# Kernel optimization log

Hardware: AMD Instinct MI355X
Metric: run time of the kernel (lower is better)

## Reference

```python
import jax, jax.numpy as jnp
import numpy as np

B, L_MAX, D, RL, RD, DOUT = 64, 4096, 128, 64, 16, 512
LN_EPS = 1e-5

def _xavier(key, shape):
    fan_in, fan_out = shape[0], shape[1]
    limit = np.sqrt(6.0 / (fan_in + fan_out)).astype(np.float32)
    return jax.random.uniform(key, shape, jnp.float32, -limit, limit)

def setup_inputs() -> dict:
    key = jax.random.key(0)
    ks = jax.random.split(key, 10)
    emb = jax.random.normal(ks[0], (B, L_MAX, D), jnp.float32)
    # contiguous padding mask from random true lengths (standard ESM padding)
    lengths = jax.random.randint(ks[1], (B,), 1, L_MAX + 1)
    mask = (jnp.arange(L_MAX)[None, :] < lengths[:, None])  # bool [B, L_max]
    B_c = _xavier(ks[2], (D, RD))
    A_c = _xavier(ks[3], (L_MAX, RL))
    H_c = _xavier(ks[4], (RL * RD, DOUT))
    W1 = _xavier(ks[5], (DOUT, DOUT))
    b1 = jnp.zeros((DOUT,), jnp.float32)
    ln_w = jnp.ones((DOUT,), jnp.float32)
    ln_b = jnp.zeros((DOUT,), jnp.float32)
    W2 = _xavier(ks[6], (DOUT, DOUT))
    b2 = jnp.zeros((DOUT,), jnp.float32)
    return {"emb": emb, "mask": mask, "B_c": B_c, "A_c": A_c, "H_c": H_c,
            "W1": W1, "b1": b1, "ln_w": ln_w, "ln_b": ln_b, "W2": W2, "b2": b2}

def reference(emb, mask, B_c, A_c, H_c, W1, b1, ln_w, ln_b, W2, b2):
    m = mask.astype(emb.dtype)                      # [B, L]
    X = emb * m[:, :, None]                         # masked embeddings [B, L, D]
    Y = jnp.einsum('bld,dr->blr', X, B_c)           # low-rank proj over D -> [B, L, rD]
    U = jnp.einsum('blr,lk->bkr', Y, A_c)           # low-rank proj over L -> [B, rL, rD]
    z = U.reshape(U.shape[0], -1) @ H_c             # [B, d]
    # expander: Linear -> LayerNorm -> ReLU -> Linear
    h = z @ W1 + b1
    mu = jnp.mean(h, axis=-1, keepdims=True)
    var = jnp.mean(jnp.square(h - mu), axis=-1, keepdims=True)
    h = (h - mu) / jnp.sqrt(var + LN_EPS) * ln_w + ln_b
    h = jax.nn.relu(h)
    return h @ W2 + b2
```

## Files before the change

kernel.cpp:

```cpp
#include <hip/hip_runtime.h>


__global__ __launch_bounds__(256) void detect_mask(
    const unsigned int* __restrict__ m, int* __restrict__ flag)
{
    unsigned int v = 0;
    int base = (blockIdx.x * 256 + threadIdx.x) * 4;
#pragma unroll
    for (int i = 0; i < 4; ++i) v |= m[base + i];
    unsigned long long any = __ballot(v > 1u);
    if ((threadIdx.x & 63) == 0 && any) atomicOr(flag, 1);
}

#define YS_STRIDE 20
#define BCS_CHUNK 516
__global__ __launch_bounds__(256, 4) void k1_proj(
    const float* __restrict__ emb,
    const void* __restrict__ maskp,
    const float* __restrict__ Bc,
    const float* __restrict__ Ac,
    float* __restrict__ Part,
    const int* __restrict__ flag)
{
    __shared__ __align__(16) float BcS[4 * BCS_CHUNK];
    __shared__ __align__(16) float As[64 * 64];
    __shared__ __align__(16) float Ys[64 * YS_STRIDE];

    const int tid  = threadIdx.x;
    const int lane = tid & 63;
    const int wave = tid >> 6;
    const int q    = tid & 3;
    const int r    = tid >> 2;
    const int b    = blockIdx.x >> 4;
    const int c    = blockIdx.x & 15;
    const int byte_mode = *flag;

#pragma unroll
    for (int i = 0; i < 8; ++i) {
        int e = i * 256 + tid;
        int k = e >> 4, col = e & 15;
        BcS[(k >> 5) * BCS_CHUNK + (k & 31) * 16 + col] = Bc[e];
    }
    __syncthreads();

    float accU[4] = {0.f, 0.f, 0.f, 0.f};

    for (int t = 0; t < 4; ++t) {
        const long l0 = (long)c * 256 + t * 64;
        const float* asrc = Ac + l0 * 64;

#pragma unroll
        for (int i = 0; i < 4; ++i) {
            int e = (i * 256 + tid) * 4;
            *(float4*)(As + e) = *(const float4*)(asrc + e);
        }

        const float* xrow = emb + ((long)b * 4096 + l0 + r) * 128 + q * 32;
        float4 xv[8];
#pragma unroll
        for (int j = 0; j < 8; ++j) xv[j] = *(const float4*)(xrow + j * 4);

        const float* bq = BcS + q * BCS_CHUNK;
        float y[16];
#pragma unroll
        for (int j = 0; j < 16; ++j) y[j] = 0.f;
#pragma unroll
        for (int j4 = 0; j4 < 8; ++j4) {
            float4 v = xv[j4];
#pragma unroll
            for (int i = 0; i < 4; ++i) {
                int kk = j4 * 4 + i;
                float x = (i == 0) ? v.x : (i == 1) ? v.y : (i == 2) ? v.z : v.w;
#pragma unroll
                for (int c4 = 0; c4 < 4; ++c4) {
                    float4 bv = *(const float4*)(bq + kk * 16 + c4 * 4);
                    y[c4 * 4 + 0] += x * bv.x;
                    y[c4 * 4 + 1] += x * bv.y;
                    y[c4 * 4 + 2] += x * bv.z;
                    y[c4 * 4 + 3] += x * bv.w;
                }
            }
        }
#pragma unroll
        for (int j = 0; j < 16; ++j) {
            y[j] += __shfl_xor(y[j], 1);
            y[j] += __shfl_xor(y[j], 2);
        }

        long midx = (long)b * 4096 + l0 + r;
        bool mb = byte_mode ? (((const unsigned char*)maskp)[midx] != 0)
                            : (((const int*)maskp)[midx] != 0);
        float mv = mb ? 1.f : 0.f;
        float4 yo;
        if (q == 0)      yo = make_float4(y[0],  y[1],  y[2],  y[3]);
        else if (q == 1) yo = make_float4(y[4],  y[5],  y[6],  y[7]);
        else if (q == 2) yo = make_float4(y[8],  y[9],  y[10], y[11]);
        else             yo = make_float4(y[12], y[13], y[14], y[15]);
        yo.x *= mv; yo.y *= mv; yo.z *= mv; yo.w *= mv;
        *(float4*)(Ys + r * YS_STRIDE + q * 4) = yo;
        __syncthreads();

        for (int l = 0; l < 64; ++l) {
            float av = As[l * 64 + lane];
            float4 yv = *(const float4*)(Ys + l * YS_STRIDE + wave * 4);
            accU[0] += av * yv.x; accU[1] += av * yv.y;
            accU[2] += av * yv.z; accU[3] += av * yv.w;
        }
        __syncthreads();
    }

    float4 uo = {accU[0], accU[1], accU[2], accU[3]};
    *(float4*)(Part + ((long)(c * 64 + b)) * 1024 + lane * 16 + wave * 4) = uo;
}

__global__ __launch_bounds__(512) void k2_fused(
    const float* __restrict__ Part,
    const float* __restrict__ Hc,
    const float* __restrict__ W1,
    const float* __restrict__ b1,
    const float* __restrict__ lnw,
    const float* __restrict__ lnb,
    const float* __restrict__ W2,
    const float* __restrict__ b2,
    float* __restrict__ out)
{
    __shared__ __align__(16) float Us[1024];
    __shared__ __align__(16) float zs[512];
    __shared__ __align__(16) float hs[512];
    __shared__ __align__(16) float hp4[4][512];
    __shared__ float red[16];

    const int tid  = threadIdx.x;
    const int lane = tid & 63;
    const int wave = tid >> 6;
    const int kq   = wave >> 1;
    const int c4   = (tid & 127) * 4;
    const int b    = blockIdx.x;

    {
        const float* pb = Part + (long)b * 1024 + tid * 2;
        float2 s = {0.f, 0.f};
#pragma unroll
        for (int cc = 0; cc < 16; ++cc) {
            float2 v = *(const float2*)(pb + (long)cc * 64 * 1024);
            s.x += v.x; s.y += v.y;
        }
        *(float2*)(Us + tid * 2) = s;
    }
    __syncthreads();

    {
        float a0 = 0.f, a1 = 0.f, a2 = 0.f, a3 = 0.f;
        const int k0 = kq * 256;
        for (int k4 = 0; k4 < 256; k4 += 4) {
            float4 u = *(const float4*)(Us + k0 + k4);
            const float* hcp = Hc + (long)(k0 + k4) * 512 + c4;
            float4 w0 = *(const float4*)(hcp);
            float4 w1v = *(const float4*)(hcp + 512);
            float4 w2v = *(const float4*)(hcp + 1024);
            float4 w3 = *(const float4*)(hcp + 1536);
            a0 += u.x * w0.x + u.y * w1v.x + u.z * w2v.x + u.w * w3.x;
            a1 += u.x * w0.y + u.y * w1v.y + u.z * w2v.y + u.w * w3.y;
            a2 += u.x * w0.z + u.y * w1v.z + u.z * w2v.z + u.w * w3.z;
            a3 += u.x * w0.w + u.y * w1v.w + u.z * w2v.w + u.w * w3.w;
        }
        float4 p = {a0, a1, a2, a3};
        *(float4*)(&hp4[kq][c4]) = p;
    }
    __syncthreads();
    if (tid < 512) {
        zs[tid] = hp4[0][tid] + hp4[1][tid] + hp4[2][tid] + hp4[3][tid];
    }
    __syncthreads();

    {
        float a0 = 0.f, a1 = 0.f, a2 = 0.f, a3 = 0.f;
        const int k0 = kq * 128;
        for (int k4 = 0; k4 < 128; k4 += 4) {
            float4 u = *(const float4*)(zs + k0 + k4);
            const float* wp = W1 + (long)(k0 + k4) * 512 + c4;
            float4 w0 = *(const float4*)(wp);
            float4 w1v = *(const float4*)(wp + 512);
            float4 w2v = *(const float4*)(wp + 1024);
            float4 w3 = *(const float4*)(wp + 1536);
            a0 += u.x * w0.x + u.y * w1v.x + u.z * w2v.x + u.w * w3.x;
            a1 += u.x * w0.y + u.y * w1v.y + u.z * w2v.y + u.w * w3.y;
            a2 += u.x * w0.z + u.y * w1v.z + u.z * w2v.z + u.w * w3.z;
            a3 += u.x * w0.w + u.y * w1v.w + u.z * w2v.w + u.w * w3.w;
        }
        float4 p = {a0, a1, a2, a3};
        *(float4*)(&hp4[kq][c4]) = p;
    }
    __syncthreads();

    float hv = hp4[0][tid] + hp4[1][tid] + hp4[2][tid] + hp4[3][tid] + b1[tid];
    float s = hv, s2 = hv * hv;
#pragma unroll
    for (int m = 32; m >= 1; m >>= 1) {
        s  += __shfl_xor(s, m);
        s2 += __shfl_xor(s2, m);
    }
    if (lane == 0) { red[wave] = s; red[wave + 8] = s2; }
    __syncthreads();
    float ts = 0.f, ts2 = 0.f;
#pragma unroll
    for (int i = 0; i < 8; ++i) { ts += red[i]; ts2 += red[i + 8]; }
    float mu   = ts * (1.f / 512.f);
    float var  = ts2 * (1.f / 512.f) - mu * mu;
    float rstd = rsqrtf(var + 1e-5f);
    float g = (hv - mu) * rstd * lnw[tid] + lnb[tid];
    hs[tid] = g > 0.f ? g : 0.f;
    __syncthreads();

    {
        float a0 = 0.f, a1 = 0.f, a2 = 0.f, a3 = 0.f;
        const int k0 = kq * 128;
        for (int k4 = 0; k4 < 128; k4 += 4) {
            float4 u = *(const float4*)(hs + k0 + k4);
            const float* wp = W2 + (long)(k0 + k4) * 512 + c4;
            float4 w0 = *(const float4*)(wp);
            float4 w1v = *(const float4*)(wp + 512);
            float4 w2v = *(const float4*)(wp + 1024);
            float4 w3 = *(const float4*)(wp + 1536);
            a0 += u.x * w0.x + u.y * w1v.x + u.z * w2v.x + u.w * w3.x;
            a1 += u.x * w0.y + u.y * w1v.y + u.z * w2v.y + u.w * w3.y;
            a2 += u.x * w0.z + u.y * w1v.z + u.z * w2v.z + u.w * w3.z;
            a3 += u.x * w0.w + u.y * w1v.w + u.z * w2v.w + u.w * w3.w;
        }
        float4 p = {a0, a1, a2, a3};
        *(float4*)(&hp4[kq][c4]) = p;
    }
    __syncthreads();
    out[(long)b * 512 + tid] = hp4[0][tid] + hp4[1][tid] + hp4[2][tid]
                             + hp4[3][tid] + b2[tid];
}

extern "C" void kernel_launch(void* const* d_in, const int* in_sizes, int n_in,
                              void* d_out, int out_size, void* d_ws, size_t ws_size,
                              hipStream_t stream) {
    const float* emb = (const float*)d_in[0];
    const void*  msk = (const void*)d_in[1];
    const float* Bc  = (const float*)d_in[2];
    const float* Ac  = (const float*)d_in[3];
    const float* Hc  = (const float*)d_in[4];
    const float* W1  = (const float*)d_in[5];
    const float* b1  = (const float*)d_in[6];
    const float* lnw = (const float*)d_in[7];
    const float* lnb = (const float*)d_in[8];
    const float* W2  = (const float*)d_in[9];
    const float* b2  = (const float*)d_in[10];

    float* Part = (float*)d_ws;
    int*   flg  = (int*)((char*)d_ws + 16 * 64 * 1024 * 4);

    hipMemsetAsync(flg, 0, 4, stream);
    detect_mask<<<64, 256, 0, stream>>>((const unsigned int*)msk, flg);
    k1_proj<<<1024, 256, 0, stream>>>(emb, msk, Bc, Ac, Part, flg);
    k2_fused<<<64, 512, 0, stream>>>(Part, Hc, W1, b1, lnw, lnb, W2, b2,
                                     (float*)d_out);
}
```

Baseline: 288.5 us.

## Split fused MLP tail into three kernels parallelized over output column quarters

Replaces the single 64-block fused head kernel (H_c projection, W1 linear, LayerNorm, ReLU, W2 linear) with three kernels of 256 blocks each. Every block handles one batch row and one quarter of the output columns. LayerNorm statistics are computed as partial sums per quarter and combined in the next kernel. The goal is to use far more CUs than 64 blocks can on MI355X, in exchange for two extra launches, global round trips for intermediate vectors, and the Part reduction being recomputed four times per batch row.

```diff
diff --git a/kernel.cpp b/kernel.cpp
--- a/kernel.cpp
+++ b/kernel.cpp
@@ -113,126 +113,186 @@
     *(float4*)(Part + ((long)(c * 64 + b)) * 1024 + lane * 16 + wave * 4) = uo;
 }
 
-__global__ __launch_bounds__(512) void k2_fused(
+__global__ __launch_bounds__(256) void k2a(
     const float* __restrict__ Part,
     const float* __restrict__ Hc,
+    float* __restrict__ zbuf)
+{
+    __shared__ __align__(16) float Us[1024];
+    __shared__ __align__(16) float hp[8][128];
+
+    const int tid = threadIdx.x;
+    const int b   = blockIdx.x >> 2;
+    const int jq  = blockIdx.x & 3;
+
+    {
+        const float* pb = Part + (long)b * 1024 + tid * 4;
+        float4 s = {0.f, 0.f, 0.f, 0.f};
+#pragma unroll
+        for (int cc = 0; cc < 16; ++cc) {
+            float4 v = *(const float4*)(pb + (long)cc * 64 * 1024);
+            s.x += v.x; s.y += v.y; s.z += v.z; s.w += v.w;
+        }
+        *(float4*)(Us + tid * 4) = s;
+    }
+    __syncthreads();
+
+    const int c4 = (tid & 31) * 4;
+    const int kq = tid >> 5;
+    const int k0 = kq * 128;
+    float a0 = 0.f, a1 = 0.f, a2 = 0.f, a3 = 0.f;
+    for (int k4 = 0; k4 < 128; k4 += 4) {
+        float4 u = *(const float4*)(Us + k0 + k4);
+        const float* hcp = Hc + (long)(k0 + k4) * 512 + jq * 128 + c4;
+        float4 w0  = *(const float4*)(hcp);
+        float4 w1v = *(const float4*)(hcp + 512);
+        float4 w2v = *(const float4*)(hcp + 1024);
+        float4 w3  = *(const float4*)(hcp + 1536);
+        a0 += u.x * w0.x + u.y * w1v.x + u.z * w2v.x + u.w * w3.x;
+        a1 += u.x * w0.y + u.y * w1v.y + u.z * w2v.y + u.w * w3.y;
+        a2 += u.x * w0.z + u.y * w1v.z + u.z * w2v.z + u.w * w3.z;
+        a3 += u.x * w0.w + u.y * w1v.w + u.z * w2v.w + u.w * w3.w;
+    }
+    float4 p = {a0, a1, a2, a3};
+    *(float4*)(&hp[kq][c4]) = p;
+    __syncthreads();
+
+    if (tid < 128) {
+        float z = hp[0][tid] + hp[1][tid] + hp[2][tid] + hp[3][tid]
+                + hp[4][tid] + hp[5][tid] + hp[6][tid] + hp[7][tid];
+        zbuf[(long)b * 512 + jq * 128 + tid] = z;
+    }
+}
+
+__global__ __launch_bounds__(256) void k2b(
+    const float* __restrict__ zbuf,
     const float* __restrict__ W1,
     const float* __restrict__ b1,
+    float* __restrict__ gbuf,
+    float* __restrict__ pstat)
+{
+    __shared__ __align__(16) float zs[512];
+    __shared__ __align__(16) float hp[8][128];
+    __shared__ float red[8];
+
+    const int tid = threadIdx.x;
+    const int b   = blockIdx.x >> 2;
+    const int jq  = blockIdx.x & 3;
+
+    if (tid < 128)
+        *(float4*)(zs + tid * 4) = *(const float4*)(zbuf + (long)b * 512 + tid * 4);
+    __syncthreads();
+
+    const int c4 = (tid & 31) * 4;
+    const int kq = tid >> 5;
+    const int k0 = kq * 64;
+    float a0 = 0.f, a1 = 0.f, a2 = 0.f, a3 = 0.f;
+    for (int k4 = 0; k4 < 64; k4 += 4) {
+        float4 u = *(const float4*)(zs + k0 + k4);
+        const float* wp = W1 + (long)(k0 + k4) * 512 + jq * 128 + c4;
+        float4 w0  = *(const float4*)(wp);
+        float4 w1v = *(const float4*)(wp + 512);
+        float4 w2v = *(const float4*)(wp + 1024);
+        float4 w3  = *(const float4*)(wp + 1536);
+        a0 += u.x * w0.x + u.y * w1v.x + u.z * w2v.x + u.w * w3.x;
+        a1 += u.x * w0.y + u.y * w1v.y + u.z * w2v.y + u.w * w3.y;
+        a2 += u.x * w0.z + u.y * w1v.z + u.z * w2v.z + u.w * w3.z;
+        a3 += u.x * w0.w + u.y * w1v.w + u.z * w2v.w + u.w * w3.w;
+    }
+    float4 p = {a0, a1, a2, a3};
+    *(float4*)(&hp[kq][c4]) = p;
+    __syncthreads();
+
+    float s = 0.f, s2 = 0.f;
+    if (tid < 128) {
+        float hv = hp[0][tid] + hp[1][tid] + hp[2][tid] + hp[3][tid]
+                 + hp[4][tid] + hp[5][tid] + hp[6][tid] + hp[7][tid]
+                 + b1[jq * 128 + tid];
+        gbuf[(long)b * 512 + jq * 128 + tid] = hv;
+        s = hv; s2 = hv * hv;
+    }
+#pragma unroll
+    for (int m = 32; m >= 1; m >>= 1) {
+        s  += __shfl_xor(s, m);
+        s2 += __shfl_xor(s2, m);
+    }
+    const int wave = tid >> 6, lane = tid & 63;
+    if (lane == 0) { red[wave] = s; red[wave + 4] = s2; }
+    __syncthreads();
+    if (tid == 0) {
+        pstat[((long)b * 4 + jq) * 2 + 0] = red[0] + red[1] + red[2] + red[3];
+        pstat[((long)b * 4 + jq) * 2 + 1] = red[4] + red[5] + red[6] + red[7];
+    }
+}
+
+__global__ __launch_bounds__(256) void k2c(
+    const float* __restrict__ gbuf,
+    const float* __restrict__ pstat,
     const float* __restrict__ lnw,
     const float* __restrict__ lnb,
     const float* __restrict__ W2,
     const float* __restrict__ b2,
     float* __restrict__ out)
 {
-    __shared__ __align__(16) float Us[1024];
-    __shared__ __align__(16) float zs[512];
     __shared__ __align__(16) float hs[512];
-    __shared__ __align__(16) float hp4[4][512];
-    __shared__ float red[16];
-
-    const int tid  = threadIdx.x;
-    const int lane = tid & 63;
-    const int wave = tid >> 6;
-    const int kq   = wave >> 1;
-    const int c4   = (tid & 127) * 4;
-    const int b    = blockIdx.x;
-
-    {
-        const float* pb = Part + (long)b * 1024 + tid * 2;
-        float2 s = {0.f, 0.f};
-#pragma unroll
-        for (int cc = 0; cc < 16; ++cc) {
-            float2 v = *(const float2*)(pb + (long)cc * 64 * 1024);
-            s.x += v.x; s.y += v.y;
-        }
-        *(float2*)(Us + tid * 2) = s;
-    }
-    __syncthreads();
-
-    {
-        float a0 = 0.f, a1 = 0.f, a2 = 0.f, a3 = 0.f;
-        const int k0 = kq * 256;
-        for (int k4 = 0; k4 < 256; k4 += 4) {
-            float4 u = *(const float4*)(Us + k0 + k4);
-            const float* hcp = Hc + (long)(k0 + k4) * 512 + c4;
-            float4 w0 = *(const float4*)(hcp);
-            float4 w1v = *(const float4*)(hcp + 512);
-            float4 w2v = *(const float4*)(hcp + 1024);
-            float4 w3 = *(const float4*)(hcp + 1536);
-            a0 += u.x * w0.x + u.y * w1v.x + u.z * w2v.x + u.w * w3.x;
-            a1 += u.x * w0.y + u.y * w1v.y + u.z * w2v.y + u.w * w3.y;
-            a2 += u.x * w0.z + u.y * w1v.z + u.z * w2v.z + u.w * w3.z;
-            a3 += u.x * w0.w + u.y * w1v.w + u.z * w2v.w + u.w * w3.w;
-        }
-        float4 p = {a0, a1, a2, a3};
-        *(float4*)(&hp4[kq][c4]) = p;
-    }
-    __syncthreads();
-    if (tid < 512) {
-        zs[tid] = hp4[0][tid] + hp4[1][tid] + hp4[2][tid] + hp4[3][tid];
-    }
-    __syncthreads();
-
-    {
-        float a0 = 0.f, a1 = 0.f, a2 = 0.f, a3 = 0.f;
-        const int k0 = kq * 128;
-        for (int k4 = 0; k4 < 128; k4 += 4) {
-            float4 u = *(const float4*)(zs + k0 + k4);
-            const float* wp = W1 + (long)(k0 + k4) * 512 + c4;
-            float4 w0 = *(const float4*)(wp);
-            float4 w1v = *(const float4*)(wp + 512);
-            float4 w2v = *(const float4*)(wp + 1024);
-            float4 w3 = *(const float4*)(wp + 1536);
-            a0 += u.x * w0.x + u.y * w1v.x + u.z * w2v.x + u.w * w3.x;
-            a1 += u.x * w0.y + u.y * w1v.y + u.z * w2v.y + u.w * w3.y;
-            a2 += u.x * w0.z + u.y * w1v.z + u.z * w2v.z + u.w * w3.z;
-            a3 += u.x * w0.w + u.y * w1v.w + u.z * w2v.w + u.w * w3.w;
-        }
-        float4 p = {a0, a1, a2, a3};
-        *(float4*)(&hp4[kq][c4]) = p;
-    }
-    __syncthreads();
-
-    float hv = hp4[0][tid] + hp4[1][tid] + hp4[2][tid] + hp4[3][tid] + b1[tid];
-    float s = hv, s2 = hv * hv;
-#pragma unroll
-    for (int m = 32; m >= 1; m >>= 1) {
-        s  += __shfl_xor(s, m);
-        s2 += __shfl_xor(s2, m);
-    }
-    if (lane == 0) { red[wave] = s; red[wave + 8] = s2; }
-    __syncthreads();
-    float ts = 0.f, ts2 = 0.f;
-#pragma unroll
-    for (int i = 0; i < 8; ++i) { ts += red[i]; ts2 += red[i + 8]; }
-    float mu   = ts * (1.f / 512.f);
-    float var  = ts2 * (1.f / 512.f) - mu * mu;
-    float rstd = rsqrtf(var + 1e-5f);
-    float g = (hv - mu) * rstd * lnw[tid] + lnb[tid];
-    hs[tid] = g > 0.f ? g : 0.f;
-    __syncthreads();
-
-    {
-        float a0 = 0.f, a1 = 0.f, a2 = 0.f, a3 = 0.f;
-        const int k0 = kq * 128;
-        for (int k4 = 0; k4 < 128; k4 += 4) {
-            float4 u = *(const float4*)(hs + k0 + k4);
-            const float* wp = W2 + (long)(k0 + k4) * 512 + c4;
-            float4 w0 = *(const float4*)(wp);
-            float4 w1v = *(const float4*)(wp + 512);
-            float4 w2v = *(const float4*)(wp + 1024);
-            float4 w3 = *(const float4*)(wp + 1536);
-            a0 += u.x * w0.x + u.y * w1v.x + u.z * w2v.x + u.w * w3.x;
-            a1 += u.x * w0.y + u.y * w1v.y + u.z * w2v.y + u.w * w3.y;
-            a2 += u.x * w0.z + u.y * w1v.z + u.z * w2v.z + u.w * w3.z;
-            a3 += u.x * w0.w + u.y * w1v.w + u.z * w2v.w + u.w * w3.w;
-        }
-        float4 p = {a0, a1, a2, a3};
-        *(float4*)(&hp4[kq][c4]) = p;
-    }
-    __syncthreads();
-    out[(long)b * 512 + tid] = hp4[0][tid] + hp4[1][tid] + hp4[2][tid]
-                             + hp4[3][tid] + b2[tid];
+    __shared__ __align__(16) float hp[8][128];
+
+    const int tid = threadIdx.x;
+    const int b   = blockIdx.x >> 2;
+    const int jq  = blockIdx.x & 3;
+
+    float S = 0.f, S2 = 0.f;
+#pragma unroll
+    for (int qq = 0; qq < 4; ++qq) {
+        S  += pstat[((long)b * 4 + qq) * 2 + 0];
+        S2 += pstat[((long)b * 4 + qq) * 2 + 1];
+    }
+    const float mu   = S * (1.f / 512.f);
+    const float var  = S2 * (1.f / 512.f) - mu * mu;
+    const float rstd = rsqrtf(var + 1e-5f);
+
+    if (tid < 128) {
+        float4 g  = *(const float4*)(gbuf + (long)b * 512 + tid * 4);
+        float4 w  = *(const float4*)(lnw + tid * 4);
+        float4 bb = *(const float4*)(lnb + tid * 4);
+        float h0 = (g.x - mu) * rstd * w.x + bb.x;
+        float h1 = (g.y - mu) * rstd * w.y + bb.y;
+        float h2 = (g.z - mu) * rstd * w.z + bb.z;
+        float h3 = (g.w - mu) * rstd * w.w + bb.w;
+        h0 = h0 > 0.f ? h0 : 0.f;
+        h1 = h1 > 0.f ? h1 : 0.f;
+        h2 = h2 > 0.f ? h2 : 0.f;
+        h3 = h3 > 0.f ? h3 : 0.f;
+        *(float4*)(hs + tid * 4) = make_float4(h0, h1, h2, h3);
+    }
+    __syncthreads();
+
+    const int c4 = (tid & 31) * 4;
+    const int kq = tid >> 5;
+    const int k0 = kq * 64;
+    float a0 = 0.f, a1 = 0.f, a2 = 0.f, a3 = 0.f;
+    for (int k4 = 0; k4 < 64; k4 += 4) {
+        float4 u = *(const float4*)(hs + k0 + k4);
+        const float* wp = W2 + (long)(k0 + k4) * 512 + jq * 128 + c4;
+        float4 w0  = *(const float4*)(wp);
+        float4 w1v = *(const float4*)(wp + 512);
+        float4 w2v = *(const float4*)(wp + 1024);
+        float4 w3  = *(const float4*)(wp + 1536);
+        a0 += u.x * w0.x + u.y * w1v.x + u.z * w2v.x + u.w * w3.x;
+        a1 += u.x * w0.y + u.y * w1v.y + u.z * w2v.y + u.w * w3.y;
+        a2 += u.x * w0.z + u.y * w1v.z + u.z * w2v.z + u.w * w3.z;
+        a3 += u.x * w0.w + u.y * w1v.w + u.z * w2v.w + u.w * w3.w;
+    }
+    float4 p = {a0, a1, a2, a3};
+    *(float4*)(&hp[kq][c4]) = p;
+    __syncthreads();
+
+    if (tid < 128) {
+        float o = hp[0][tid] + hp[1][tid] + hp[2][tid] + hp[3][tid]
+                + hp[4][tid] + hp[5][tid] + hp[6][tid] + hp[7][tid]
+                + b2[jq * 128 + tid];
+        out[(long)b * 512 + jq * 128 + tid] = o;
+    }
 }
 
 extern "C" void kernel_launch(void* const* d_in, const int* in_sizes, int n_in,
@@ -250,12 +310,16 @@
     const float* W2  = (const float*)d_in[9];
     const float* b2  = (const float*)d_in[10];
 
-    float* Part = (float*)d_ws;
-    int*   flg  = (int*)((char*)d_ws + 16 * 64 * 1024 * 4);
+    float* Part  = (float*)d_ws;
+    int*   flg   = (int*)((char*)d_ws + 4 * 1024 * 1024);
+    float* zbuf  = (float*)((char*)d_ws + 4 * 1024 * 1024 + 4096);
+    float* gbuf  = zbuf + 64 * 512;
+    float* pstat = gbuf + 64 * 512;
 
     hipMemsetAsync(flg, 0, 4, stream);
     detect_mask<<<64, 256, 0, stream>>>((const unsigned int*)msk, flg);
     k1_proj<<<1024, 256, 0, stream>>>(emb, msk, Bc, Ac, Part, flg);
-    k2_fused<<<64, 512, 0, stream>>>(Part, Hc, W1, b1, lnw, lnb, W2, b2,
-                                     (float*)d_out);
-}
+    k2a<<<256, 256, 0, stream>>>(Part, Hc, zbuf);
+    k2b<<<256, 256, 0, stream>>>(zbuf, W1, b1, gbuf, pstat);
+    k2c<<<256, 256, 0, stream>>>(gbuf, pstat, lnw, lnb, W2, b2, (float*)d_out);
+}
```

After: 260.7 us. -9.6%, faster.
